# Kernel optimization log

Hardware: AMD Instinct MI355X
Metric: run time of the kernel (lower is better)

Reference implementation:

```python
import jax, jax.numpy as jnp
import numpy as np

SPARSITY_A = 0.1
SPARSITY_B = 0.5

N, L, C = 8, 8192, 3


def setup_inputs() -> dict:
    key = jax.random.key(0)
    k1, k2, k3, k4 = jax.random.split(key, 4)
    inp = jax.random.normal(k1, (N, L, C), dtype=jnp.float32)
    tgt = jax.random.uniform(k2, (N, L, C), dtype=jnp.float32)
    class_weights = jax.random.uniform(k3, (C,), dtype=jnp.float32) + 0.5
    pos_weight = jax.random.uniform(k4, (C,), dtype=jnp.float32) * 4.0 + 1.0
    return {"input": inp, "target": tgt, "class_weights": class_weights, "pos_weight": pos_weight}


def _proximity(s1, s2):
    # full cross-correlation (length 2L-1), same set of values as torch conv1d w/ padding=L-1
    cc = jnp.convolve(s1, s2[::-1], mode="full")
    e1 = jnp.sum(s1 * s1)
    e2 = jnp.sum(s2 * s2)
    norm = jnp.sqrt(e1 * e2)
    penalty = 1.0 - jnp.sqrt(e1 + e2) / norm
    return (cc / norm + penalty).mean()


def _sparsity(x):
    # NOTE: original code does x[1:] - x[:1] (diff vs FIRST element), preserved here.
    # x: (N, L, C-1) -> (N, C-1)
    d = x[:, 1:, :] - x[:, :1, :]
    return SPARSITY_A * jnp.sum(jnp.abs(d) - SPARSITY_B * jnp.maximum(d, 0.0), axis=1)


def reference(input, target, class_weights, pos_weight):
    # --- weighted BCE-with-logits per channel ---
    log_sig = jax.nn.log_sigmoid(input)      # (N,L,C)
    log_one_minus = jax.nn.log_sigmoid(-input)
    bce = -(pos_weight * target * log_sig + (1.0 - target) * log_one_minus)
    bce_per_c = bce.mean(axis=(0, 1))        # (C,)
    loss = jnp.sum(10.0 * class_weights * bce_per_c)

    # --- proximity between channels 1 and 2, per batch element ---
    prox = jax.vmap(_proximity)(input[:, :, 1], input[:, :, 2])  # (N,)
    loss = loss + jnp.sum(prox)

    # --- sparsity loss over channels 1..C-1, per batch element ---
    s_in = _sparsity(input[:, :, 1:])    # (N, C-1)
    s_tg = _sparsity(target[:, :, 1:])   # (N, C-1)
    loss = loss + jnp.sum(jnp.abs(s_in - s_tg) / (s_tg + 1.0))
    return loss
```

## Files before the change

### kernel.cpp

```cpp
#include <hip/hip_runtime.h>
#include <math.h>

#define LEN 8192
#define NBATCH 8
#define NCH 3
#define BLK 256
#define BPN (LEN / BLK)
#define NBLOCKS (NBATCH * BPN)
#define NQ 11


__device__ __forceinline__ float log_sigmoid(float x) {
    return fminf(x, 0.0f) - log1pf(expf(-fabsf(x)));
}

__device__ __forceinline__ float sp_term(float d) {
    return fabsf(d) - 0.5f * fmaxf(d, 0.0f);
}

__global__ __launch_bounds__(BLK) void partial_kernel(
        const float* __restrict__ inp,
        const float* __restrict__ tgt,
        const float* __restrict__ pw,
        float* __restrict__ part) {
    const int b = blockIdx.x;
    const int n = b >> 5;
    const int l = ((b & 31) << 8) + threadIdx.x;
    const float* ip = inp + (size_t)n * LEN * NCH;
    const float* tp = tgt + (size_t)n * LEN * NCH;

    const float x0 = ip[l * 3 + 0];
    const float x1 = ip[l * 3 + 1];
    const float x2 = ip[l * 3 + 2];
    const float t0 = tp[l * 3 + 0];
    const float t1 = tp[l * 3 + 1];
    const float t2 = tp[l * 3 + 2];

    const float bi1 = ip[1], bi2 = ip[2];
    const float bt1 = tp[1], bt2 = tp[2];

    const float pw0 = pw[0], pw1 = pw[1], pw2 = pw[2];

    float v[NQ];
    {
        float ls0 = log_sigmoid(x0), ln0 = log_sigmoid(-x0);
        float ls1 = log_sigmoid(x1), ln1 = log_sigmoid(-x1);
        float ls2 = log_sigmoid(x2), ln2 = log_sigmoid(-x2);
        v[0] = -(pw0 * t0 * ls0 + (1.0f - t0) * ln0);
        v[1] = -(pw1 * t1 * ls1 + (1.0f - t1) * ln1);
        v[2] = -(pw2 * t2 * ls2 + (1.0f - t2) * ln2);
    }
    v[3] = x1;
    v[4] = x2;
    v[5] = x1 * x1;
    v[6] = x2 * x2;
    v[7]  = sp_term(x1 - bi1);
    v[8]  = sp_term(x2 - bi2);
    v[9]  = sp_term(t1 - bt1);
    v[10] = sp_term(t2 - bt2);

    __shared__ float red[4][NQ];
    const int lane = threadIdx.x & 63;
    const int wv   = threadIdx.x >> 6;
#pragma unroll
    for (int q = 0; q < NQ; ++q) {
        float s = v[q];
#pragma unroll
        for (int off = 32; off >= 1; off >>= 1) s += __shfl_down(s, off, 64);
        if (lane == 0) red[wv][q] = s;
    }
    __syncthreads();
    if (threadIdx.x < NQ) {
        const int q = threadIdx.x;
        part[b * NQ + q] = red[0][q] + red[1][q] + red[2][q] + red[3][q];
    }
}

__global__ __launch_bounds__(BLK) void finalize_kernel(
        const float* __restrict__ part,
        const float* __restrict__ cw,
        float* __restrict__ out) {
    const int t = threadIdx.x;
    float v[NQ];
#pragma unroll
    for (int q = 0; q < NQ; ++q) v[q] = part[t * NQ + q];

    const int lane = t & 63;
    const int wv   = t >> 6;
    __shared__ float bceS[4][3];
    __shared__ float perN[NBATCH][8];

#pragma unroll
    for (int q = 0; q < 3; ++q) {
        float s = v[q];
#pragma unroll
        for (int off = 32; off >= 1; off >>= 1) s += __shfl_down(s, off, 64);
        if (lane == 0) bceS[wv][q] = s;
    }
#pragma unroll
    for (int q = 3; q < NQ; ++q) {
        float s = v[q];
#pragma unroll
        for (int off = 16; off >= 1; off >>= 1) s += __shfl_down(s, off, 32);
        if ((t & 31) == 0) perN[t >> 5][q - 3] = s;
    }
    __syncthreads();

    if (t == 0) {
        float loss = 0.0f;
        const float invNL = 1.0f / (float)(NBATCH * LEN);
#pragma unroll
        for (int c = 0; c < 3; ++c) {
            float s = bceS[0][c] + bceS[1][c] + bceS[2][c] + bceS[3][c];
            loss += 10.0f * cw[c] * (s * invNL);
        }
#pragma unroll
        for (int n = 0; n < NBATCH; ++n) {
            const float sum1 = perN[n][0], sum2 = perN[n][1];
            const float e1   = perN[n][2], e2   = perN[n][3];
            const float norm = sqrtf(e1 * e2);
            loss += (sum1 * sum2) / (norm * (float)(2 * LEN - 1))
                    + 1.0f - sqrtf(e1 + e2) / norm;
#pragma unroll
            for (int c = 0; c < 2; ++c) {
                const float si = 0.1f * perN[n][4 + c];
                const float st = 0.1f * perN[n][6 + c];
                loss += fabsf(si - st) / (st + 1.0f);
            }
        }
        out[0] = loss;
    }
}

extern "C" void kernel_launch(void* const* d_in, const int* in_sizes, int n_in,
                              void* d_out, int out_size, void* d_ws, size_t ws_size,
                              hipStream_t stream) {
    const float* inp = (const float*)d_in[0];
    const float* tgt = (const float*)d_in[1];
    const float* cw  = (const float*)d_in[2];
    const float* pw  = (const float*)d_in[3];
    float* part = (float*)d_ws;

    partial_kernel<<<NBLOCKS, BLK, 0, stream>>>(inp, tgt, pw, part);
    finalize_kernel<<<1, BLK, 0, stream>>>(part, cw, (float*)d_out);
}
```

Baseline: 67.17 us.

## Fuse partial and finalize kernels with last-block atomic counter and float4 loads

Merges the two-kernel reduction into one kernel: each block writes its partial sums, increments a global counter, and the last block to finish performs the final reduction and loss computation. Each thread now handles four positions using vectorized float4 loads, which cuts the block count from 256 to 64. The BCE expression is also rewritten to need one log-sigmoid per element instead of two. A memset launch is added to reset the counter, and the kernel now depends on threadfence and atomic ordering to be correct.

```diff
diff --git a/kernel.cpp b/kernel.cpp
--- a/kernel.cpp
+++ b/kernel.cpp
@@ -5,7 +5,8 @@
 #define NBATCH 8
 #define NCH 3
 #define BLK 256
-#define BPN (LEN / BLK)
+#define PPT 4
+#define BPN (LEN / (BLK * PPT))
 #define NBLOCKS (NBATCH * BPN)
 #define NQ 11
 
@@ -18,46 +19,54 @@
     return fabsf(d) - 0.5f * fmaxf(d, 0.0f);
 }
 
-__global__ __launch_bounds__(BLK) void partial_kernel(
+__global__ __launch_bounds__(BLK) void fused_kernel(
         const float* __restrict__ inp,
         const float* __restrict__ tgt,
+        const float* __restrict__ cw,
         const float* __restrict__ pw,
-        float* __restrict__ part) {
+        unsigned int* __restrict__ counter,
+        float* __restrict__ part,
+        float* __restrict__ out) {
     const int b = blockIdx.x;
-    const int n = b >> 5;
-    const int l = ((b & 31) << 8) + threadIdx.x;
+    const int n = b >> 3;
+    const int l0 = (((b & 7) << 8) + threadIdx.x) * PPT;
     const float* ip = inp + (size_t)n * LEN * NCH;
     const float* tp = tgt + (size_t)n * LEN * NCH;
 
-    const float x0 = ip[l * 3 + 0];
-    const float x1 = ip[l * 3 + 1];
-    const float x2 = ip[l * 3 + 2];
-    const float t0 = tp[l * 3 + 0];
-    const float t1 = tp[l * 3 + 1];
-    const float t2 = tp[l * 3 + 2];
-
     const float bi1 = ip[1], bi2 = ip[2];
     const float bt1 = tp[1], bt2 = tp[2];
-
     const float pw0 = pw[0], pw1 = pw[1], pw2 = pw[2];
 
+    const float4* i4 = reinterpret_cast<const float4*>(ip + (size_t)l0 * NCH);
+    const float4* t4 = reinterpret_cast<const float4*>(tp + (size_t)l0 * NCH);
+    const float4 ia = i4[0], ib = i4[1], ic = i4[2];
+    const float4 ta = t4[0], tb = t4[1], tc = t4[2];
+
+    const float xs[PPT][3] = {{ia.x, ia.y, ia.z}, {ia.w, ib.x, ib.y},
+                              {ib.z, ib.w, ic.x}, {ic.y, ic.z, ic.w}};
+    const float tss[PPT][3] = {{ta.x, ta.y, ta.z}, {ta.w, tb.x, tb.y},
+                               {tb.z, tb.w, tc.x}, {tc.y, tc.z, tc.w}};
+
     float v[NQ];
-    {
-        float ls0 = log_sigmoid(x0), ln0 = log_sigmoid(-x0);
-        float ls1 = log_sigmoid(x1), ln1 = log_sigmoid(-x1);
-        float ls2 = log_sigmoid(x2), ln2 = log_sigmoid(-x2);
-        v[0] = -(pw0 * t0 * ls0 + (1.0f - t0) * ln0);
-        v[1] = -(pw1 * t1 * ls1 + (1.0f - t1) * ln1);
-        v[2] = -(pw2 * t2 * ls2 + (1.0f - t2) * ln2);
+#pragma unroll
+    for (int q = 0; q < NQ; ++q) v[q] = 0.0f;
+
+#pragma unroll
+    for (int p = 0; p < PPT; ++p) {
+        const float x0 = xs[p][0], x1 = xs[p][1], x2 = xs[p][2];
+        const float t0 = tss[p][0], t1 = tss[p][1], t2 = tss[p][2];
+        v[0] += (1.0f - t0) * x0 - (pw0 * t0 + 1.0f - t0) * log_sigmoid(x0);
+        v[1] += (1.0f - t1) * x1 - (pw1 * t1 + 1.0f - t1) * log_sigmoid(x1);
+        v[2] += (1.0f - t2) * x2 - (pw2 * t2 + 1.0f - t2) * log_sigmoid(x2);
+        v[3] += x1;
+        v[4] += x2;
+        v[5] += x1 * x1;
+        v[6] += x2 * x2;
+        v[7]  += sp_term(x1 - bi1);
+        v[8]  += sp_term(x2 - bi2);
+        v[9]  += sp_term(t1 - bt1);
+        v[10] += sp_term(t2 - bt2);
     }
-    v[3] = x1;
-    v[4] = x2;
-    v[5] = x1 * x1;
-    v[6] = x2 * x2;
-    v[7]  = sp_term(x1 - bi1);
-    v[8]  = sp_term(x2 - bi2);
-    v[9]  = sp_term(t1 - bt1);
-    v[10] = sp_term(t2 - bt2);
 
     __shared__ float red[4][NQ];
     const int lane = threadIdx.x & 63;
@@ -70,61 +79,61 @@
         if (lane == 0) red[wv][q] = s;
     }
     __syncthreads();
-    if (threadIdx.x < NQ) {
-        const int q = threadIdx.x;
-        part[b * NQ + q] = red[0][q] + red[1][q] + red[2][q] + red[3][q];
+
+    __shared__ int lastFlag;
+    if (threadIdx.x == 0) {
+#pragma unroll
+        for (int q = 0; q < NQ; ++q)
+            part[b * NQ + q] = red[0][q] + red[1][q] + red[2][q] + red[3][q];
+        __threadfence();
+        unsigned int old = atomicAdd(counter, 1u);
+        lastFlag = (old == NBLOCKS - 1);
     }
-}
+    __syncthreads();
+    if (!lastFlag) return;
 
-__global__ __launch_bounds__(BLK) void finalize_kernel(
-        const float* __restrict__ part,
-        const float* __restrict__ cw,
-        float* __restrict__ out) {
-    const int t = threadIdx.x;
-    float v[NQ];
+    __threadfence();
+    __shared__ float bceS[3];
+    __shared__ float perN[NBATCH][8];
+    if (threadIdx.x < 64) {
+        volatile const float* vp = part + threadIdx.x * NQ;
+        float r[NQ];
 #pragma unroll
-    for (int q = 0; q < NQ; ++q) v[q] = part[t * NQ + q];
-
-    const int lane = t & 63;
-    const int wv   = t >> 6;
-    __shared__ float bceS[4][3];
-    __shared__ float perN[NBATCH][8];
-
+        for (int q = 0; q < NQ; ++q) r[q] = vp[q];
 #pragma unroll
-    for (int q = 0; q < 3; ++q) {
-        float s = v[q];
+        for (int q = 0; q < 3; ++q) {
+            float s = r[q];
 #pragma unroll
-        for (int off = 32; off >= 1; off >>= 1) s += __shfl_down(s, off, 64);
-        if (lane == 0) bceS[wv][q] = s;
-    }
+            for (int off = 32; off >= 1; off >>= 1) s += __shfl_down(s, off, 64);
+            if (threadIdx.x == 0) bceS[q] = s;
+        }
 #pragma unroll
-    for (int q = 3; q < NQ; ++q) {
-        float s = v[q];
+        for (int q = 3; q < NQ; ++q) {
+            float s = r[q];
 #pragma unroll
-        for (int off = 16; off >= 1; off >>= 1) s += __shfl_down(s, off, 32);
-        if ((t & 31) == 0) perN[t >> 5][q - 3] = s;
+            for (int off = 4; off >= 1; off >>= 1) s += __shfl_down(s, off, 8);
+            if ((threadIdx.x & 7) == 0) perN[threadIdx.x >> 3][q - 3] = s;
+        }
     }
     __syncthreads();
 
-    if (t == 0) {
+    if (threadIdx.x == 0) {
         float loss = 0.0f;
         const float invNL = 1.0f / (float)(NBATCH * LEN);
 #pragma unroll
-        for (int c = 0; c < 3; ++c) {
-            float s = bceS[0][c] + bceS[1][c] + bceS[2][c] + bceS[3][c];
-            loss += 10.0f * cw[c] * (s * invNL);
-        }
+        for (int c = 0; c < 3; ++c)
+            loss += 10.0f * cw[c] * (bceS[c] * invNL);
 #pragma unroll
-        for (int n = 0; n < NBATCH; ++n) {
-            const float sum1 = perN[n][0], sum2 = perN[n][1];
-            const float e1   = perN[n][2], e2   = perN[n][3];
+        for (int n2 = 0; n2 < NBATCH; ++n2) {
+            const float sum1 = perN[n2][0], sum2 = perN[n2][1];
+            const float e1   = perN[n2][2], e2   = perN[n2][3];
             const float norm = sqrtf(e1 * e2);
             loss += (sum1 * sum2) / (norm * (float)(2 * LEN - 1))
                     + 1.0f - sqrtf(e1 + e2) / norm;
 #pragma unroll
             for (int c = 0; c < 2; ++c) {
-                const float si = 0.1f * perN[n][4 + c];
-                const float st = 0.1f * perN[n][6 + c];
+                const float si = 0.1f * perN[n2][4 + c];
+                const float st = 0.1f * perN[n2][6 + c];
                 loss += fabsf(si - st) / (st + 1.0f);
             }
         }
@@ -139,8 +148,11 @@
     const float* tgt = (const float*)d_in[1];
     const float* cw  = (const float*)d_in[2];
     const float* pw  = (const float*)d_in[3];
-    float* part = (float*)d_ws;
 
-    partial_kernel<<<NBLOCKS, BLK, 0, stream>>>(inp, tgt, pw, part);
-    finalize_kernel<<<1, BLK, 0, stream>>>(part, cw, (float*)d_out);
+    unsigned int* counter = (unsigned int*)d_ws;
+    float* part = (float*)((char*)d_ws + 256);
+
+    hipMemsetAsync(counter, 0, sizeof(unsigned int), stream);
+    fused_kernel<<<NBLOCKS, BLK, 0, stream>>>(inp, tgt, cw, pw,
+                                              counter, part, (float*)d_out);
 }
```

Result: slower. 73.46 us (+9.4%).
